# Kernel tuning notes

Hardware: AMD Instinct MI355X
Metric: run time of the kernel (lower is better)

Reference implementation:

```python
import jax, jax.numpy as jnp
import numpy as np

M_FEATS = 1536      # number of proposals (docstring: [M, K])
K_DIM = 128         # feature dim per docstring example
NUM_CLASSES = 16    # label vocabulary; torch.unique loop becomes a fixed class sweep


def setup_inputs() -> dict:
    key = jax.random.key(0)
    k1, k2 = jax.random.split(key)
    features = jax.random.normal(k1, (M_FEATS, K_DIM), dtype=jnp.float32)
    labels = jax.random.randint(k2, (M_FEATS,), 0, NUM_CLASSES, dtype=jnp.int32)
    # ious all ones -> keep = (ious >= 0.5) is all-True, so the boolean filter is identity
    ious = jnp.ones((M_FEATS,), dtype=jnp.float32)
    return {"features": features, "labels": labels, "ious": ious}


def reference(features, labels, ious):
    # reweight_func='none' -> coef = ones_like(ious); keep mask is all-True by construction
    coef = jnp.ones_like(ious)
    # similarity [M, M]; coef broadcasts over columns, matching `similarity * coef` in torch
    sim = jnp.matmul(features, features.T) * coef[None, :]
    m = sim.shape[0]
    eye = jnp.eye(m, dtype=sim.dtype)
    # ground set term: logdet(similarity + 0.5 I)  (mask_ground is all ones)
    ground = jnp.linalg.slogdet(sim + 0.5 * eye)[1]

    # Per-label logdet of the submatrix S_c + 0.5 I_{n_c}. Instead of extracting a
    # variable-size submatrix (not jit-able), embed it in a full [M, M] matrix that is
    # block-diagonal: class block = S_c + 0.5 I, off-class diagonal = 1. Its logdet
    # equals logdet(S_c + 0.5 I). Absent classes give identity -> logdet 0, matching
    # torch.unique skipping them.
    onehot = (labels[:, None] == jnp.arange(NUM_CLASSES, dtype=labels.dtype)[None, :])
    onehot = onehot.astype(sim.dtype)  # [M, C]

    def class_logdet(mask):  # mask: [M] 0/1 indicator for one class
        A = sim * (mask[:, None] * mask[None, :]) + jnp.diag(0.5 * mask + (1.0 - mask))
        return jnp.linalg.slogdet(A)[1]

    per_class = jax.vmap(class_logdet)(onehot.T)  # [C]
    loss = jnp.sum(per_class) - ground
    return loss  # scalar; .mean() of a scalar is itself
```

## Files before the change

### kernel.cpp

```cpp
#include <hip/hip_runtime.h>
#include <math.h>


#define M_FEATS 1536
#define K_DIM 128
#define NUM_CLASSES 16
#define GRAM_ELEMS (K_DIM * K_DIM)
#define SENT 0x13579BDF
#define MP 104
#define WS2 40

typedef short bf16x8 __attribute__((ext_vector_type(8)));
typedef float f32x4 __attribute__((ext_vector_type(4)));

__device__ __forceinline__ short f2bf(float x) {
    unsigned u = __float_as_uint(x);
    u += 0x7FFFu + ((u >> 16) & 1u);
    return (short)(u >> 16);
}

__device__ __forceinline__ float chol128_acc(
    const int t,
    f32x4 a0, f32x4 a1, f32x4 a2, f32x4 a3,
    f32x4 a4, f32x4 a5, f32x4 a6, f32x4 a7,
    float* __restrict__ strip, short* __restrict__ Whl, float* __restrict__ logp)
{
    const int wave = t >> 6, lane = t & 63, ln = lane & 15, quad = lane >> 4;

#pragma unroll 1
    for (int s = 0; s < 16; ++s) {
        const int k = 8 * s;

        const int sw = s >> 1, sq = (s & 1) * 2;
        if (wave == sw && (quad == sq || quad == sq + 1)) {
            float* sp = strip + (quad - sq) * 4 + ln * 8;
            *(f32x4*)(sp + 0)   = a0; *(f32x4*)(sp + 128) = a1;
            *(f32x4*)(sp + 256) = a2; *(f32x4*)(sp + 384) = a3;
            *(f32x4*)(sp + 512) = a4; *(f32x4*)(sp + 640) = a5;
            *(f32x4*)(sp + 768) = a6; *(f32x4*)(sp + 896) = a7;
        }
        __syncthreads();

        if (t < K_DIM) {
            float D[8][8];
#pragma unroll
            for (int c = 0; c < 8; ++c) {
                float4 d0 = *(const float4*)(strip + (k + c) * 8);
                float4 d1 = *(const float4*)(strip + (k + c) * 8 + 4);
                D[0][c] = d0.x; D[1][c] = d0.y; D[2][c] = d0.z; D[3][c] = d0.w;
                D[4][c] = d1.x; D[5][c] = d1.y; D[6][c] = d1.z; D[7][c] = d1.w;
            }
            float4 av0 = *(const float4*)(strip + t * 8);
            float4 av1 = *(const float4*)(strip + t * 8 + 4);
            float a[8] = {av0.x, av0.y, av0.z, av0.w, av1.x, av1.y, av1.z, av1.w};

            float L[8][8], ic[8];
            float prod = 1.0f;
#pragma unroll
            for (int c = 0; c < 8; ++c) {
                float v = D[c][c];
#pragma unroll
                for (int m = 0; m < c; ++m) v = fmaf(-L[c][m], L[c][m], v);
                prod *= v;
                ic[c] = rsqrtf(v);
#pragma unroll
                for (int r = c + 1; r < 8; ++r) {
                    float x = D[r][c];
#pragma unroll
                    for (int m = 0; m < c; ++m) x = fmaf(-L[r][m], L[c][m], x);
                    L[r][c] = x * ic[c];
                }
            }
            if (t == 0) logp[s] = prod;

            float w[8];
#pragma unroll
            for (int c = 0; c < 8; ++c) {
                float x = a[c];
#pragma unroll
                for (int m = 0; m < c; ++m) x = fmaf(-L[c][m], w[m], x);
                w[c] = x * ic[c];
            }
            if (t < k) {
#pragma unroll
                for (int c = 0; c < 8; ++c) w[c] = 0.f;
            }

            unsigned uh[4], ul[4];
#pragma unroll
            for (int j = 0; j < 4; ++j) {
                const float w0 = w[2 * j], w1 = w[2 * j + 1];
                const unsigned h0 = (unsigned short)f2bf(w0);
                const unsigned h1 = (unsigned short)f2bf(w1);
                const float f0 = __uint_as_float(h0 << 16);
                const float f1 = __uint_as_float(h1 << 16);
                const unsigned l0 = (unsigned short)f2bf(w0 - f0);
                const unsigned l1 = (unsigned short)f2bf(w1 - f1);
                uh[j] = (h1 << 16) | h0;
                ul[j] = (l1 << 16) | l0;
            }
            short* wp = Whl + t * WS2;
            *(int4*)(wp) = make_int4((int)uh[0], (int)uh[1], (int)uh[2], (int)uh[3]);
            *(int4*)(wp + 8) = make_int4((int)ul[0], (int)ul[1], (int)ul[2], (int)ul[3]);
            *(int4*)(wp + 16) = make_int4((int)(uh[0] ^ 0x80008000u), (int)(uh[1] ^ 0x80008000u),
                                          (int)(uh[2] ^ 0x80008000u), (int)(uh[3] ^ 0x80008000u));
            *(int4*)(wp + 24) = make_int4((int)(ul[0] ^ 0x80008000u), (int)(ul[1] ^ 0x80008000u),
                                          (int)(ul[2] ^ 0x80008000u), (int)(ul[3] ^ 0x80008000u));
        }
        __syncthreads();

        const int live = 8 * (s + 1);
        if ((wave * 16 + 16) > live) {
            const bf16x8 z = {};
            bf16x8 fa = *(const bf16x8*)(Whl + ((wave * 16 + ln) * WS2) + (quad & 1) * 8);
            fa = (quad < 2) ? fa : z;
#define TRAIL_TC(TC) \
            if ((TC * 16 + 16) > live) { \
                const short* bp = Whl + (TC * 16 + ln) * WS2; \
                bf16x8 bh = *(const bf16x8*)(bp + 16); \
                bf16x8 bl = *(const bf16x8*)(bp + 24); \
                bh = (quad < 2) ? bh : z; \
                bl = (quad < 2) ? bl : z; \
                a##TC = __builtin_amdgcn_mfma_f32_16x16x32_bf16(fa, bh, a##TC, 0, 0, 0); \
                a##TC = __builtin_amdgcn_mfma_f32_16x16x32_bf16(fa, bl, a##TC, 0, 0, 0); \
            }
            TRAIL_TC(0) TRAIL_TC(1) TRAIL_TC(2) TRAIL_TC(3)
            TRAIL_TC(4) TRAIL_TC(5) TRAIL_TC(6) TRAIL_TC(7)
#undef TRAIL_TC
        }
    }

    float ls = 0.0f;
    if (t == 0) {
#pragma unroll
        for (int ss = 0; ss < 16; ++ss) ls += logf(logp[ss]);
    }
    return ls;
}

__global__ __launch_bounds__(512, 1) void fused_kernel(
    const float* __restrict__ f, const int* __restrict__ labels,
    float* __restrict__ groundG, float* __restrict__ ldet,
    int* __restrict__ flagG, int* __restrict__ flag3,
    float* __restrict__ out)
{
    __shared__ int cnt;
    __shared__ int list[M_FEATS];
    __shared__ __align__(16) short FT[K_DIM * MP];
    __shared__ __align__(16) float strip[8 * 128];
    __shared__ __align__(16) short Whl[K_DIM * WS2];
    __shared__ float logp[16];

    const int b = blockIdx.x;
    const int t = threadIdx.x;
    const int wave = t >> 6, lane = t & 63, ln = lane & 15, quad = lane >> 4;

#define DECL8(P) \
    f32x4 P##0 = (f32x4){0.f,0.f,0.f,0.f}, P##1 = (f32x4){0.f,0.f,0.f,0.f}, \
          P##2 = (f32x4){0.f,0.f,0.f,0.f}, P##3 = (f32x4){0.f,0.f,0.f,0.f}, \
          P##4 = (f32x4){0.f,0.f,0.f,0.f}, P##5 = (f32x4){0.f,0.f,0.f,0.f}, \
          P##6 = (f32x4){0.f,0.f,0.f,0.f}, P##7 = (f32x4){0.f,0.f,0.f,0.f}
#define FOR8(OP) OP(g0,0) OP(g1,1) OP(g2,2) OP(g3,3) OP(g4,4) OP(g5,5) OP(g6,6) OP(g7,7)
#define DIAGADD(VAR, TC) \
    if (wave == TC) { \
        if (ln == quad * 4 + 0) VAR[0] += 0.5f; \
        else if (ln == quad * 4 + 1) VAR[1] += 0.5f; \
        else if (ln == quad * 4 + 2) VAR[2] += 0.5f; \
        else if (ln == quad * 4 + 3) VAR[3] += 0.5f; }

    if (b < NUM_CLASSES) {
        const int cls = b;
        if (t == 0) cnt = 0;
        __syncthreads();
        {
            const unsigned long long ltmask = (lane == 63)
                ? 0x7FFFFFFFFFFFFFFFull : ((1ull << lane) - 1ull);
#pragma unroll
            for (int it = 0; it < M_FEATS / 512; ++it) {
                const int i = it * 512 + t;
                const bool pred = (labels[i] == cls);
                const unsigned long long mask = __ballot(pred);
                int base = 0;
                if (lane == 0 && mask)
                    base = atomicAdd(&cnt, __popcll(mask));
                base = __shfl(base, 0);
                if (pred)
                    list[base + __popcll(mask & ltmask)] = i;
            }
        }
        __syncthreads();
        const int n = cnt;

        DECL8(g);

        const int mlane = t & 31, cgrp = t >> 5;
        const int nchunks = (n + 95) / 96;
        for (int ch = 0; ch < nchunks; ++ch) {
            const int cb = ch * 96;
            const int live = n - cb;
            const int kcmax = (live >= 96) ? 3 : ((live + 31) >> 5);
#pragma unroll
            for (int it = 0; it < 6; ++it) {
                const int mg = it % 3;
                if (mg >= kcmax) continue;
                const int m = mg * 32 + mlane;
                const int cgp = (it / 3) * 16 + cgrp;
                const int gm = cb + m;
                float4 v = make_float4(0.f, 0.f, 0.f, 0.f);
                if (gm < n) {
                    const int src = list[gm];
                    v = *(const float4*)(f + (size_t)src * K_DIM + cgp * 4);
                }
                FT[(cgp * 4 + 0) * MP + m] = f2bf(v.x);
                FT[(cgp * 4 + 1) * MP + m] = f2bf(v.y);
                FT[(cgp * 4 + 2) * MP + m] = f2bf(v.z);
                FT[(cgp * 4 + 3) * MP + m] = f2bf(v.w);
            }
            __syncthreads();
            for (int kc = 0; kc < kcmax; ++kc) {
                const int kb = kc * 32 + quad * 8;
                const bf16x8 fa = *(const bf16x8*)(FT + (wave * 16 + ln) * MP + kb);
#define GRAM_TC(TC) { \
                const bf16x8 bb = *(const bf16x8*)(FT + (TC * 16 + ln) * MP + kb); \
                g##TC = __builtin_amdgcn_mfma_f32_16x16x32_bf16(fa, bb, g##TC, 0, 0, 0); }
                GRAM_TC(0) GRAM_TC(1) GRAM_TC(2) GRAM_TC(3)
                GRAM_TC(4) GRAM_TC(5) GRAM_TC(6) GRAM_TC(7)
#undef GRAM_TC
            }
            __syncthreads();
        }

#define SCAT(VAR, TC) { \
        const int row0 = wave * 16 + quad * 4; \
        const int col = TC * 16 + ln; \
        unsafeAtomicAdd(&groundG[(row0 + 0) * K_DIM + col], VAR[0]); \
        unsafeAtomicAdd(&groundG[(row0 + 1) * K_DIM + col], VAR[1]); \
        unsafeAtomicAdd(&groundG[(row0 + 2) * K_DIM + col], VAR[2]); \
        unsafeAtomicAdd(&groundG[(row0 + 3) * K_DIM + col], VAR[3]); }
        FOR8(SCAT)
#undef SCAT
        __syncthreads();
        if (t == 0)
            __hip_atomic_store(&flagG[cls], SENT, __ATOMIC_RELEASE,
                               __HIP_MEMORY_SCOPE_AGENT);

        FOR8(DIAGADD)

        float ls = chol128_acc(t, g0, g1, g2, g3, g4, g5, g6, g7,
                               strip, Whl, logp);

        if (t == 0) {
            ldet[cls] = ls;
            __hip_atomic_store(&flag3[cls], SENT, __ATOMIC_RELEASE,
                               __HIP_MEMORY_SCOPE_AGENT);
        }
        return;
    }

    if (t < NUM_CLASSES)
        while (__hip_atomic_load(&flagG[t], __ATOMIC_ACQUIRE,
                                 __HIP_MEMORY_SCOPE_AGENT) != SENT)
            __builtin_amdgcn_s_sleep(2);
    __syncthreads();

    DECL8(g);
#define LOADG(VAR, TC) { \
    const int row0 = wave * 16 + quad * 4; \
    const int col = TC * 16 + ln; \
    VAR = (f32x4){groundG[(row0 + 0) * K_DIM + col], \
                  groundG[(row0 + 1) * K_DIM + col], \
                  groundG[(row0 + 2) * K_DIM + col], \
                  groundG[(row0 + 3) * K_DIM + col]}; }
    FOR8(LOADG)
#undef LOADG
    FOR8(DIAGADD)

    float ls = chol128_acc(t, g0, g1, g2, g3, g4, g5, g6, g7,
                           strip, Whl, logp);

    if (t < NUM_CLASSES)
        while (__hip_atomic_load(&flag3[t], __ATOMIC_ACQUIRE,
                                 __HIP_MEMORY_SCOPE_AGENT) != SENT)
            __builtin_amdgcn_s_sleep(2);
    __syncthreads();

    if (t == 0) {
        float total = 1920.0f * 0.6931471805599453f - ls;
#pragma unroll
        for (int c = 0; c < NUM_CLASSES; ++c) total += ldet[c];
        out[0] = total;
    }
}

extern "C" void kernel_launch(void* const* d_in, const int* in_sizes, int n_in,
                              void* d_out, int out_size, void* d_ws, size_t ws_size,
                              hipStream_t stream)
{
    const float* features = (const float*)d_in[0];
    const int* labels = (const int*)d_in[1];

    float* groundG = (float*)d_ws;
    float* ldetp   = groundG + GRAM_ELEMS;
    int* flagG     = (int*)(ldetp + NUM_CLASSES);
    int* flag3     = flagG + NUM_CLASSES;

    fused_kernel<<<NUM_CLASSES + 1, 512, 0, stream>>>(
        features, labels, groundG, ldetp, flagG, flag3, (float*)d_out);
}
```

Baseline: 86.54 us.

## Replace per-step block barriers in Cholesky with LDS flag-based wave synchronization

Replaces the two __syncthreads per panel step of the blocked 128x128 Cholesky with workgroup-scope LDS counters and flags. The W panel buffer is double-buffered, so the two panel-factorizing waves can start the next step as soon as its strip is dumped, without waiting for all waves. The goal is to cut barrier stalls and overlap panel factorization with trailing MFMA updates. In exchange it adds spin-wait polling and a risk of subtle ordering bugs in strip reuse, since the strip is overwritten while other waves may still be reading it.

```diff
diff --git a/kernel.cpp b/kernel.cpp
--- a/kernel.cpp
+++ b/kernel.cpp
@@ -13,6 +13,10 @@
 typedef short bf16x8 __attribute__((ext_vector_type(8)));
 typedef float f32x4 __attribute__((ext_vector_type(4)));
 
+#define LDS_LOAD_ACQ(P)  __hip_atomic_load((P), __ATOMIC_ACQUIRE, __HIP_MEMORY_SCOPE_WORKGROUP)
+#define LDS_ADD_REL(P)   __hip_atomic_fetch_add((P), 1, __ATOMIC_RELEASE, __HIP_MEMORY_SCOPE_WORKGROUP)
+#define LDS_STORE_REL(P) __hip_atomic_store((P), 1, __ATOMIC_RELEASE, __HIP_MEMORY_SCOPE_WORKGROUP)
+
 __device__ __forceinline__ short f2bf(float x) {
     unsigned u = __float_as_uint(x);
     u += 0x7FFFu + ((u >> 16) & 1u);
@@ -23,25 +27,34 @@
     const int t,
     f32x4 a0, f32x4 a1, f32x4 a2, f32x4 a3,
     f32x4 a4, f32x4 a5, f32x4 a6, f32x4 a7,
-    float* __restrict__ strip, short* __restrict__ Whl, float* __restrict__ logp)
+    float* __restrict__ strip, short* __restrict__ Whl, float* __restrict__ logp,
+    int* __restrict__ fS, int* __restrict__ cdone, int* __restrict__ tdone)
 {
     const int wave = t >> 6, lane = t & 63, ln = lane & 15, quad = lane >> 4;
+
+    if (t < 16) { fS[t] = 0; cdone[t] = 0; tdone[t] = 0; }
+    __syncthreads();
+
+#define DUMP_STRIP(SQ) { \
+    float* sp = strip + (quad - (SQ)) * 4 + ln * 8;    \
+    *(f32x4*)(sp + 0)   = a0; *(f32x4*)(sp + 128) = a1; \
+    *(f32x4*)(sp + 256) = a2; *(f32x4*)(sp + 384) = a3; \
+    *(f32x4*)(sp + 512) = a4; *(f32x4*)(sp + 640) = a5; \
+    *(f32x4*)(sp + 768) = a6; *(f32x4*)(sp + 896) = a7; }
+
+    if (wave == 0 && quad <= 1) DUMP_STRIP(0)
+    if (t == 0) LDS_STORE_REL(&fS[0]);
 
 #pragma unroll 1
     for (int s = 0; s < 16; ++s) {
         const int k = 8 * s;
-
-        const int sw = s >> 1, sq = (s & 1) * 2;
-        if (wave == sw && (quad == sq || quad == sq + 1)) {
-            float* sp = strip + (quad - sq) * 4 + ln * 8;
-            *(f32x4*)(sp + 0)   = a0; *(f32x4*)(sp + 128) = a1;
-            *(f32x4*)(sp + 256) = a2; *(f32x4*)(sp + 384) = a3;
-            *(f32x4*)(sp + 512) = a4; *(f32x4*)(sp + 640) = a5;
-            *(f32x4*)(sp + 768) = a6; *(f32x4*)(sp + 896) = a7;
-        }
-        __syncthreads();
+        short* WB = Whl + (s & 1) * (K_DIM * WS2);
 
         if (t < K_DIM) {
+            while (LDS_LOAD_ACQ(&fS[s]) != 1) __builtin_amdgcn_s_sleep(1);
+            if (s >= 2)
+                while (LDS_LOAD_ACQ(&tdone[s - 2]) != 8) __builtin_amdgcn_s_sleep(1);
+
             float D[8][8];
 #pragma unroll
             for (int c = 0; c < 8; ++c) {
@@ -99,24 +112,26 @@
                 uh[j] = (h1 << 16) | h0;
                 ul[j] = (l1 << 16) | l0;
             }
-            short* wp = Whl + t * WS2;
+            short* wp = WB + t * WS2;
             *(int4*)(wp) = make_int4((int)uh[0], (int)uh[1], (int)uh[2], (int)uh[3]);
             *(int4*)(wp + 8) = make_int4((int)ul[0], (int)ul[1], (int)ul[2], (int)ul[3]);
             *(int4*)(wp + 16) = make_int4((int)(uh[0] ^ 0x80008000u), (int)(uh[1] ^ 0x80008000u),
                                           (int)(uh[2] ^ 0x80008000u), (int)(uh[3] ^ 0x80008000u));
             *(int4*)(wp + 24) = make_int4((int)(ul[0] ^ 0x80008000u), (int)(ul[1] ^ 0x80008000u),
                                           (int)(ul[2] ^ 0x80008000u), (int)(ul[3] ^ 0x80008000u));
-        }
-        __syncthreads();
+            if (lane == 0) LDS_ADD_REL(&cdone[s]);
+        }
+
+        while (LDS_LOAD_ACQ(&cdone[s]) != 2) __builtin_amdgcn_s_sleep(1);
 
         const int live = 8 * (s + 1);
         if ((wave * 16 + 16) > live) {
             const bf16x8 z = {};
-            bf16x8 fa = *(const bf16x8*)(Whl + ((wave * 16 + ln) * WS2) + (quad & 1) * 8);
+            bf16x8 fa = *(const bf16x8*)(WB + ((wave * 16 + ln) * WS2) + (quad & 1) * 8);
             fa = (quad < 2) ? fa : z;
 #define TRAIL_TC(TC) \
             if ((TC * 16 + 16) > live) { \
-                const short* bp = Whl + (TC * 16 + ln) * WS2; \
+                const short* bp = WB + (TC * 16 + ln) * WS2; \
                 bf16x8 bh = *(const bf16x8*)(bp + 16); \
                 bf16x8 bl = *(const bf16x8*)(bp + 24); \
                 bh = (quad < 2) ? bh : z; \
@@ -128,7 +143,15 @@
             TRAIL_TC(4) TRAIL_TC(5) TRAIL_TC(6) TRAIL_TC(7)
 #undef TRAIL_TC
         }
+
+        if (s < 15) {
+            const int ow = (s + 1) >> 1, oq = ((s + 1) & 1) * 2;
+            if (wave == ow && (quad == oq || quad == oq + 1)) DUMP_STRIP(oq)
+            if (wave == ow && lane == 0) LDS_STORE_REL(&fS[s + 1]);
+        }
+        if (lane == 0) LDS_ADD_REL(&tdone[s]);
     }
+#undef DUMP_STRIP
 
     float ls = 0.0f;
     if (t == 0) {
@@ -148,8 +171,9 @@
     __shared__ int list[M_FEATS];
     __shared__ __align__(16) short FT[K_DIM * MP];
     __shared__ __align__(16) float strip[8 * 128];
-    __shared__ __align__(16) short Whl[K_DIM * WS2];
+    __shared__ __align__(16) short Whl[2 * K_DIM * WS2];
     __shared__ float logp[16];
+    __shared__ int fS[16], cdone[16], tdone[16];
 
     const int b = blockIdx.x;
     const int t = threadIdx.x;
@@ -197,8 +221,8 @@
         const int nchunks = (n + 95) / 96;
         for (int ch = 0; ch < nchunks; ++ch) {
             const int cb = ch * 96;
-            const int live = n - cb;
-            const int kcmax = (live >= 96) ? 3 : ((live + 31) >> 5);
+            const int lv = n - cb;
+            const int kcmax = (lv >= 96) ? 3 : ((lv + 31) >> 5);
 #pragma unroll
             for (int it = 0; it < 6; ++it) {
                 const int mg = it % 3;
@@ -247,7 +271,7 @@
         FOR8(DIAGADD)
 
         float ls = chol128_acc(t, g0, g1, g2, g3, g4, g5, g6, g7,
-                               strip, Whl, logp);
+                               strip, Whl, logp, fS, cdone, tdone);
 
         if (t == 0) {
             ldet[cls] = ls;
@@ -276,7 +300,7 @@
     FOR8(DIAGADD)
 
     float ls = chol128_acc(t, g0, g1, g2, g3, g4, g5, g6, g7,
-                           strip, Whl, logp);
+                           strip, Whl, logp, fS, cdone, tdone);
 
     if (t < NUM_CLASSES)
         while (__hip_atomic_load(&flag3[t], __ATOMIC_ACQUIRE,
```

Measured after the change: 89.56 us. 3.5% more time.
